# Kernel tuning notes

Hardware: AMD Instinct MI355X
Metric: run time of the kernel (lower is better)

## Reference

```python
import jax, jax.numpy as jnp
import numpy as np

EPS = 1e-6
N_HEADS = 16


def _inner(x, y):
    # Lorentzian inner product: -x0*y0 + <x_space, y_space>
    return -x[..., 0] * y[..., 0] + jnp.sum(x[..., 1:] * y[..., 1:], axis=-1)


def _project(x):
    sp = jnp.clip(x[..., 1:], -8.0, 8.0)
    x0 = jnp.sqrt(1.0 + jnp.sum(sp ** 2, axis=-1, keepdims=True) + EPS)
    return jnp.concatenate([x0, sp], axis=-1)


def _exp_map(x, v):
    vx = _inner(v, x)[..., None]
    v_tan = v + vx * x
    v_ns = jnp.maximum(_inner(v_tan, v_tan), 0.0)
    v_n = jnp.minimum(jnp.sqrt(v_ns + EPS)[..., None], 5.0)
    res = jnp.cosh(v_n) * x + jnp.sinh(v_n) * v_tan / (v_n + EPS)
    return _project(res)


def _log_map(x, y):
    y = _project(y)
    xy = jnp.minimum(_inner(x, y)[..., None], -(1.0 + EPS))
    d = jnp.maximum(jnp.arccosh(jnp.maximum(-xy, 1.0 + EPS)), 0.001)
    direc = y + xy * x
    dn = jnp.sqrt(jnp.maximum(_inner(direc, direc), EPS))[..., None]
    return d * direc / (dn + EPS)


def setup_inputs() -> dict:
    key = jax.random.key(0)
    ks = jax.random.split(key, 5)
    B, T, d = 2, 1024, 1024
    x = jax.random.normal(ks[0], (B, T, d), dtype=jnp.float32)
    s = 0.02
    Wq = jax.random.normal(ks[1], (d, d), dtype=jnp.float32) * s
    Wk = jax.random.normal(ks[2], (d, d), dtype=jnp.float32) * s
    Wv = jax.random.normal(ks[3], (d, d), dtype=jnp.float32) * s
    Wo = jax.random.normal(ks[4], (d, d), dtype=jnp.float32) * s
    return {"x": x, "Wq": Wq, "Wk": Wk, "Wv": Wv, "Wo": Wo}


def reference(x, Wq, Wk, Wv, Wo):
    B, T, d = x.shape
    h = N_HEADS
    dh = d // h
    mu = jnp.zeros((d,), dtype=x.dtype).at[0].set(1.0)  # hyperboloid origin

    v = _log_map(mu, x)  # [B, T, d]

    def proj_h(w):
        hh = w.reshape(B, T, h, dh)
        sp = jnp.clip(hh[..., 1:], -5.0, 5.0)
        x0 = jnp.sqrt(1.0 + jnp.sum(sp ** 2, axis=-1, keepdims=True) + EPS)
        return jnp.transpose(jnp.concatenate([x0, sp], axis=-1), (0, 2, 1, 3))  # [B,h,T,dh]

    q = proj_h(v @ Wq.T)
    k = proj_h(v @ Wk.T)
    vv = jnp.transpose((v @ Wv.T).reshape(B, T, h, dh), (0, 2, 1, 3))  # [B,h,T,dh]

    # Lorentzian scores: -q0*k0 + <q_space, k_space>
    sc = (-jnp.einsum("bhqi,bhki->bhqk", q[..., :1], k[..., :1])
          + jnp.einsum("bhqc,bhkc->bhqk", q[..., 1:], k[..., 1:])) / (dh ** 0.5)
    at = jax.nn.softmax(sc, axis=-1)
    out = jnp.einsum("bhqk,bhkc->bhqc", at, vv)
    out = jnp.transpose(out, (0, 2, 1, 3)).reshape(B, T, d)
    return _project(_exp_map(mu, out @ Wo.T))
```

## Files before the change

kernel.cpp:

```cpp
#include <hip/hip_runtime.h>

#define EPSF 1e-6f

typedef __bf16 bf16x8 __attribute__((ext_vector_type(8)));
typedef float f32x4 __attribute__((ext_vector_type(4)));
typedef __attribute__((address_space(3))) unsigned int as3_uint;
typedef __attribute__((address_space(1))) const unsigned int as1_uint;

__device__ __forceinline__ unsigned short f2bf(float f) {
  unsigned int u = __builtin_bit_cast(unsigned int, f);
  u += 0x7fffu + ((u >> 16) & 1u);
  return (unsigned short)(u >> 16);
}
__device__ __forceinline__ float bf2f(unsigned short u) {
  unsigned int v = (unsigned int)u << 16;
  return __builtin_bit_cast(float, v);
}

__global__ __launch_bounds__(256) void prep_and_conv(
    const float* __restrict__ x, const float* __restrict__ Wq,
    const float* __restrict__ Wk, const float* __restrict__ Wv,
    const float* __restrict__ Wo, unsigned short* __restrict__ vbf,
    unsigned short* __restrict__ wqk, unsigned short* __restrict__ wvb,
    unsigned short* __restrict__ wob) {
  int bid = blockIdx.x;
  int tid = threadIdx.x;
  if (bid >= 2048) {
    int t = bid - 2048;
    int y = t >> 10;
    const float* src = (y == 0) ? Wq : (y == 1) ? Wk : (y == 2) ? Wv : Wo;
    unsigned short* dst = (y == 0) ? wqk : (y == 1) ? wqk + 1048576
                          : (y == 2) ? wvb : wob;
    int i = (t & 1023) * 256 + tid;
    f32x4 v = ((const f32x4*)src)[i];
    ushort4 o;
    o.x = f2bf(v[0]); o.y = f2bf(v[1]); o.z = f2bf(v[2]); o.w = f2bf(v[3]);
    ((ushort4*)dst)[i] = o;
    return;
  }
  int row = bid;
  const float* xr = x + (size_t)row * 1024;
  float vals[4];
  float ssq = 0.f;
#pragma unroll
  for (int i = 0; i < 4; ++i) {
    int c = tid + i * 256;
    float t = xr[c];
    if (c == 0) {
      vals[i] = 0.f;
    } else {
      t = fminf(fmaxf(t, -8.f), 8.f);
      vals[i] = t;
      ssq += t * t;
    }
  }
#pragma unroll
  for (int off = 32; off; off >>= 1) ssq += __shfl_xor(ssq, off);
  __shared__ float red[4];
  int wv = tid >> 6;
  if ((tid & 63) == 0) red[wv] = ssq;
  __syncthreads();
  ssq = red[0] + red[1] + red[2] + red[3];

  float y0 = sqrtf(1.f + ssq + EPSF);
  float xy = fminf(-y0, -(1.f + EPSF));
  float mxy = fmaxf(-xy, 1.f + EPSF);
  float dd = fmaxf(acoshf(mxy), 0.001f);
  float d0 = y0 + xy;
  float inn = ssq - d0 * d0;
  float dn = sqrtf(fmaxf(inn, EPSF));
  float inv = dd / (dn + EPSF);

  unsigned short* vr = vbf + (size_t)row * 1024;
#pragma unroll
  for (int i = 0; i < 4; ++i) {
    int c = tid + i * 256;
    float o = (c == 0) ? d0 * inv : vals[i] * inv;
    vr[c] = f2bf(o);
  }
}

__device__ __forceinline__ void gemm128_body(
    const unsigned short* __restrict__ A, const unsigned short* __restrict__ Bw,
    int K, int row0, int col0, unsigned short* As, unsigned short* Bs,
    f32x4 (*acc)[4]) {
  int tid = threadIdx.x;
  int lane = tid & 63, w = tid >> 6;
  int wm = (w >> 1) * 64, wn = (w & 1) * 64;
  int lq = lane & 15, g = lane >> 4;
  const unsigned short* Ag =
      A + (size_t)(row0 + w * 8 + (lane >> 3)) * K + (lane & 7) * 8;
  const unsigned short* Bg =
      Bw + (size_t)(col0 + w * 8 + (lane >> 3)) * K + (lane & 7) * 8;

  for (int k0 = 0; k0 < K; k0 += 64) {
    __syncthreads();
#pragma unroll
    for (int it = 0; it < 4; ++it) {
      __builtin_amdgcn_global_load_lds(
          (as1_uint*)(Ag + (size_t)(it * 32) * K + k0),
          (as3_uint*)&As[(it * 32 + w * 8) * 64], 16, 0, 0);
      __builtin_amdgcn_global_load_lds(
          (as1_uint*)(Bg + (size_t)(it * 32) * K + k0),
          (as3_uint*)&Bs[(it * 32 + w * 8) * 64], 16, 0, 0);
    }
    __syncthreads();
#pragma unroll
    for (int ks = 0; ks < 2; ++ks) {
      bf16x8 af[4], bfr[4];
#pragma unroll
      for (int i = 0; i < 4; ++i)
        af[i] = *(const bf16x8*)&As[(wm + i * 16 + lq) * 64 + ks * 32 + g * 8];
#pragma unroll
      for (int j = 0; j < 4; ++j)
        bfr[j] = *(const bf16x8*)&Bs[(wn + j * 16 + lq) * 64 + ks * 32 + g * 8];
#pragma unroll
      for (int i = 0; i < 4; ++i)
#pragma unroll
        for (int j = 0; j < 4; ++j)
          acc[i][j] =
              __builtin_amdgcn_mfma_f32_16x16x32_bf16(af[i], bfr[j], acc[i][j], 0, 0, 0);
    }
  }
}

__global__ __launch_bounds__(256) void gemm_qkv(
    const unsigned short* __restrict__ vbf, const unsigned short* __restrict__ wqk,
    const unsigned short* __restrict__ wvb, unsigned short* __restrict__ qb,
    unsigned short* __restrict__ kb, unsigned short* __restrict__ vtb) {
  __shared__ unsigned short As[128 * 64];
  __shared__ unsigned short Bs[128 * 64];
  f32x4 acc[4][4] = {};
  int tid = threadIdx.x;
  int lane = tid & 63, w = tid >> 6;
  int wm = (w >> 1) * 64, wn = (w & 1) * 64;
  int lq = lane & 15, g = lane >> 4;
  int bid = blockIdx.x;

  if (bid < 256) {
    int row0 = (bid & 15) * 128, col0 = (bid >> 4) * 128;
    gemm128_body(vbf, wqk, 1024, row0, col0, As, Bs, acc);
    int headg = (col0 + wn) >> 6;
    int qmode = (headg < 16) ? 1 : 0;
    unsigned short* dst = qmode ? qb : kb;
    size_t colb = (size_t)(headg & 15) * 64;
    float scale = qmode ? 0.125f : 1.f;
#pragma unroll
    for (int i = 0; i < 4; ++i)
#pragma unroll
      for (int r = 0; r < 4; ++r) {
        float s = 0.f;
#pragma unroll
        for (int j = 0; j < 4; ++j) {
          float vc = fminf(fmaxf(acc[i][j][r], -5.f), 5.f);
          s += (j == 0 && lq == 0) ? 0.f : vc * vc;
        }
        s += __shfl_xor(s, 1);
        s += __shfl_xor(s, 2);
        s += __shfl_xor(s, 4);
        s += __shfl_xor(s, 8);
        float x0 = sqrtf(1.f + s + EPSF);
        int row = row0 + wm + i * 16 + g * 4 + r;
#pragma unroll
        for (int j = 0; j < 4; ++j) {
          float vc = fminf(fmaxf(acc[i][j][r], -5.f), 5.f);
          float o = (j == 0 && lq == 0) ? (qmode ? -x0 : x0) : vc;
          dst[(size_t)row * 1024 + colb + j * 16 + lq] = f2bf(o * scale);
        }
      }
  } else {
    int t = bid - 256;
    int row0 = (t & 7) * 128, col0 = (t >> 3) * 128;
    gemm128_body(wvb, vbf, 1024, row0, col0, As, Bs, acc);
#pragma unroll
    for (int i = 0; i < 4; ++i)
#pragma unroll
      for (int j = 0; j < 4; ++j)
#pragma unroll
        for (int r = 0; r < 4; ++r)
          vtb[(size_t)(row0 + wm + i * 16 + g * 4 + r) * 2048 + col0 + wn + j * 16 + lq] =
              f2bf(acc[i][j][r]);
  }
}

__global__ __launch_bounds__(256) void gemm_wo(
    const unsigned short* __restrict__ A, const unsigned short* __restrict__ Bw,
    unsigned short* __restrict__ C) {
  __shared__ unsigned short As[128 * 64];
  __shared__ unsigned short Bs[128 * 64];
  f32x4 acc[4][4] = {};
  int bid = blockIdx.x;
  int row0 = (bid & 15) * 128, col0 = (bid >> 4) * 128;
  gemm128_body(A, Bw, 1024, row0, col0, As, Bs, acc);
  int tid = threadIdx.x;
  int lane = tid & 63, w = tid >> 6;
  int wm = (w >> 1) * 64, wn = (w & 1) * 64;
  int lq = lane & 15, g = lane >> 4;
#pragma unroll
  for (int i = 0; i < 4; ++i)
#pragma unroll
    for (int j = 0; j < 4; ++j)
#pragma unroll
      for (int r = 0; r < 4; ++r)
        C[(size_t)(row0 + wm + i * 16 + g * 4 + r) * 1024 + col0 + wn + j * 16 + lq] =
            f2bf(acc[i][j][r]);
}

__global__ __launch_bounds__(256) void attn_mfma(
    const unsigned short* __restrict__ Qb, const unsigned short* __restrict__ Kb,
    const unsigned short* __restrict__ Vtb, unsigned short* __restrict__ Obf) {
  __shared__ unsigned short Ks[2][64 * 64];
  __shared__ unsigned short Vs[2][64 * 64];
  __shared__ unsigned short Ps[4 * 16 * 64];
  int tid = threadIdx.x;
  int lane = tid & 63, w = tid >> 6;
  int g = lane >> 4, lq = lane & 15;
  int bh = blockIdx.x >> 4, qt = blockIdx.x & 15;
  int b = bh >> 4, h = bh & 15;

  const unsigned short* qrow =
      Qb + (size_t)(b * 1024 + qt * 64 + w * 16 + lq) * 1024 + h * 64;
  bf16x8 qf0 = *(const bf16x8*)(qrow + g * 8);
  bf16x8 qf1 = *(const bf16x8*)(qrow + 32 + g * 8);

  float mreg = -1e30f, lreg = 0.f;
  f32x4 acc[4] = {};
  unsigned short* Pw = Ps + w * 16 * 64;
  int sx = 8 * (lq & 7);

  const unsigned short* Ksrc = Kb + (size_t)(b * 1024) * 1024 + h * 64;
  const unsigned short* Vsrc = Vtb + (size_t)(h * 64) * 2048 + b * 1024;

  int srow = lane >> 3;
  int scg = (lane & 7) ^ srow;
  const unsigned short* Kp = Ksrc + (size_t)(w * 8 + srow) * 1024 + scg * 8;
  const unsigned short* Vp = Vsrc + (size_t)(w * 8 + srow) * 2048 + scg * 8;

  auto stage = [&](int buf, int kt) {
#pragma unroll
    for (int it = 0; it < 2; ++it) {
      __builtin_amdgcn_global_load_lds(
          (as1_uint*)(Kp + (size_t)(kt * 64 + it * 32) * 1024),
          (as3_uint*)&Ks[buf][(it * 32 + w * 8) * 64], 16, 0, 0);
      __builtin_amdgcn_global_load_lds(
          (as1_uint*)(Vp + (size_t)(it * 32) * 2048 + kt * 64),
          (as3_uint*)&Vs[buf][(it * 32 + w * 8) * 64], 16, 0, 0);
    }
  };

  auto compute = [&](int buf) {
    f32x4 st[4];
#pragma unroll
    for (int i = 0; i < 4; ++i) {
      int ro = i * 16 + lq;
      int rb = ro * 64, xx = 8 * (ro & 7);
      bf16x8 a0 = *(const bf16x8*)&Ks[buf][rb + ((g * 8) ^ xx)];
      bf16x8 a1 = *(const bf16x8*)&Ks[buf][rb + ((32 + g * 8) ^ xx)];
      f32x4 z = {};
      z = __builtin_amdgcn_mfma_f32_16x16x32_bf16(a0, qf0, z, 0, 0, 0);
      st[i] = __builtin_amdgcn_mfma_f32_16x16x32_bf16(a1, qf1, z, 0, 0, 0);
    }
    float pmax = st[0][0];
#pragma unroll
    for (int i = 0; i < 4; ++i)
#pragma unroll
      for (int r = 0; r < 4; ++r) pmax = fmaxf(pmax, st[i][r]);
    pmax = fmaxf(pmax, __shfl_xor(pmax, 16));
    pmax = fmaxf(pmax, __shfl_xor(pmax, 32));
    float nm = fmaxf(mreg, pmax);
    float sc_ = __expf(mreg - nm);
    mreg = nm;
    float ps = 0.f;
#pragma unroll
    for (int i = 0; i < 4; ++i) {
      ushort4 pq;
      float p0 = __expf(st[i][0] - nm);
      float p1 = __expf(st[i][1] - nm);
      float p2 = __expf(st[i][2] - nm);
      float p3 = __expf(st[i][3] - nm);
      ps += (p0 + p1) + (p2 + p3);
      pq.x = f2bf(p0); pq.y = f2bf(p1); pq.z = f2bf(p2); pq.w = f2bf(p3);
      *(ushort4*)&Pw[lq * 64 + ((g * 4 + i * 16) ^ sx)] = pq;
    }
    ps += __shfl_xor(ps, 16);
    ps += __shfl_xor(ps, 32);
    lreg = lreg * sc_ + ps;

    float scr[4];
#pragma unroll
    for (int r = 0; r < 4; ++r) scr[r] = __shfl(sc_, g * 4 + r);
#pragma unroll
    for (int jj = 0; jj < 4; ++jj)
#pragma unroll
      for (int r = 0; r < 4; ++r) acc[jj][r] *= scr[r];
#pragma unroll
    for (int ks = 0; ks < 2; ++ks) {
      bf16x8 pa = *(const bf16x8*)&Pw[lq * 64 + ((ks * 32 + g * 8) ^ sx)];
#pragma unroll
      for (int jj = 0; jj < 4; ++jj) {
        int vr = 16 * jj + lq;
        bf16x8 vb = *(const bf16x8*)&Vs[buf][vr * 64 + ((ks * 32 + g * 8) ^ (8 * (vr & 7)))];
        acc[jj] = __builtin_amdgcn_mfma_f32_16x16x32_bf16(pa, vb, acc[jj], 0, 0, 0);
      }
    }
  };

  stage(0, 0);
  int buf = 0;
  for (int kt = 0; kt < 16; ++kt) {
    __syncthreads();
    if (kt + 1 < 16) stage(buf ^ 1, kt + 1);
    compute(buf);
    buf ^= 1;
  }

  float linv = 1.f / lreg;
  float ilr[4];
#pragma unroll
  for (int r = 0; r < 4; ++r) ilr[r] = __shfl(linv, g * 4 + r);
  unsigned short* obase =
      Obf + (size_t)(b * 1024 + qt * 64 + w * 16) * 1024 + h * 64;
#pragma unroll
  for (int r = 0; r < 4; ++r)
#pragma unroll
    for (int jj = 0; jj < 4; ++jj)
      obase[(size_t)(g * 4 + r) * 1024 + 16 * jj + lq] = f2bf(acc[jj][r] * ilr[r]);
}

__global__ __launch_bounds__(256) void expmap_project(
    const unsigned short* __restrict__ c2, float* __restrict__ out) {
  int row = blockIdx.x;
  int tid = threadIdx.x;
  const unsigned short* cr = c2 + (size_t)row * 1024;
  float vals[4];
  float ssq = 0.f;
#pragma unroll
  for (int i = 0; i < 4; ++i) {
    int c = tid + i * 256;
    float t = bf2f(cr[c]);
    vals[i] = (c == 0) ? 0.f : t;
    ssq += vals[i] * vals[i];
  }
#pragma unroll
  for (int off = 32; off; off >>= 1) ssq += __shfl_xor(ssq, off);
  __shared__ float red1[4], red2[4];
  int wv = tid >> 6;
  if ((tid & 63) == 0) red1[wv] = ssq;
  __syncthreads();
  ssq = red1[0] + red1[1] + red1[2] + red1[3];
  float vn = fminf(sqrtf(ssq + EPSF), 5.f);
  float bf = sinhf(vn) / (vn + EPSF);
  float s2 = 0.f;
#pragma unroll
  for (int i = 0; i < 4; ++i) {
    float r = fminf(fmaxf(bf * vals[i], -8.f), 8.f);
    vals[i] = r;
    s2 += r * r;
  }
#pragma unroll
  for (int off = 32; off; off >>= 1) s2 += __shfl_xor(s2, off);
  if ((tid & 63) == 0) red2[wv] = s2;
  __syncthreads();
  s2 = red2[0] + red2[1] + red2[2] + red2[3];
  float x0 = sqrtf(1.f + s2 + EPSF);
  float* orow = out + (size_t)row * 1024;
#pragma unroll
  for (int i = 0; i < 4; ++i) {
    int c = tid + i * 256;
    orow[c] = (c == 0) ? x0 : vals[i];
  }
}

extern "C" void kernel_launch(void* const* d_in, const int* in_sizes, int n_in,
                              void* d_out, int out_size, void* d_ws, size_t ws_size,
                              hipStream_t stream) {
  (void)in_sizes; (void)n_in; (void)out_size; (void)ws_size;
  const float* x  = (const float*)d_in[0];
  const float* Wq = (const float*)d_in[1];
  const float* Wk = (const float*)d_in[2];
  const float* Wv = (const float*)d_in[3];
  const float* Wo = (const float*)d_in[4];
  float* out = (float*)d_out;

  char* w = (char*)d_ws;
  unsigned short* vbf = (unsigned short*)w; w += (size_t)2048 * 1024 * 2;
  unsigned short* wqk = (unsigned short*)w; w += (size_t)2048 * 1024 * 2;
  unsigned short* wvb = (unsigned short*)w; w += (size_t)1024 * 1024 * 2;
  unsigned short* wob = (unsigned short*)w; w += (size_t)1024 * 1024 * 2;
  unsigned short* vtb = (unsigned short*)w; w += (size_t)1024 * 2048 * 2;
  unsigned short* qb  = (unsigned short*)w; w += (size_t)2048 * 1024 * 2;
  unsigned short* kb  = (unsigned short*)w; w += (size_t)2048 * 1024 * 2;
  unsigned short* aob = (unsigned short*)w; w += (size_t)2048 * 1024 * 2;
  unsigned short* c2  = (unsigned short*)w; w += (size_t)2048 * 1024 * 2;

  prep_and_conv<<<6144, 256, 0, stream>>>(x, Wq, Wk, Wv, Wo, vbf, wqk, wvb, wob);

  gemm_qkv<<<384, 256, 0, stream>>>(vbf, wqk, wvb, qb, kb, vtb);

  attn_mfma<<<512, 256, 0, stream>>>(qb, kb, vtb, aob);

  gemm_wo<<<128, 256, 0, stream>>>(aob, wob, c2);
  expmap_project<<<2048, 256, 0, stream>>>(c2, out);
}
```

Measured before the change: 93.23 us.

## Retile Wo GEMM to 128x64, lazy softmax rescale, setprio and block remap in attention

```diff
diff --git a/kernel.cpp b/kernel.cpp
--- a/kernel.cpp
+++ b/kernel.cpp
@@ -187,19 +187,52 @@
     const unsigned short* __restrict__ A, const unsigned short* __restrict__ Bw,
     unsigned short* __restrict__ C) {
   __shared__ unsigned short As[128 * 64];
-  __shared__ unsigned short Bs[128 * 64];
-  f32x4 acc[4][4] = {};
-  int bid = blockIdx.x;
-  int row0 = (bid & 15) * 128, col0 = (bid >> 4) * 128;
-  gemm128_body(A, Bw, 1024, row0, col0, As, Bs, acc);
+  __shared__ unsigned short Bs[64 * 64];
   int tid = threadIdx.x;
   int lane = tid & 63, w = tid >> 6;
-  int wm = (w >> 1) * 64, wn = (w & 1) * 64;
+  int wm = (w >> 1) * 64, wn = (w & 1) * 32;
   int lq = lane & 15, g = lane >> 4;
+  int row0 = (blockIdx.x & 15) * 128, col0 = (blockIdx.x >> 4) * 64;
+  f32x4 acc[4][2] = {};
+  const unsigned short* Ag =
+      A + (size_t)(row0 + w * 8 + (lane >> 3)) * 1024 + (lane & 7) * 8;
+  const unsigned short* Bg =
+      Bw + (size_t)(col0 + w * 8 + (lane >> 3)) * 1024 + (lane & 7) * 8;
+
+  for (int k0 = 0; k0 < 1024; k0 += 64) {
+    __syncthreads();
+#pragma unroll
+    for (int it = 0; it < 4; ++it)
+      __builtin_amdgcn_global_load_lds(
+          (as1_uint*)(Ag + (size_t)(it * 32) * 1024 + k0),
+          (as3_uint*)&As[(it * 32 + w * 8) * 64], 16, 0, 0);
+#pragma unroll
+    for (int it = 0; it < 2; ++it)
+      __builtin_amdgcn_global_load_lds(
+          (as1_uint*)(Bg + (size_t)(it * 32) * 1024 + k0),
+          (as3_uint*)&Bs[(it * 32 + w * 8) * 64], 16, 0, 0);
+    __syncthreads();
+#pragma unroll
+    for (int ks = 0; ks < 2; ++ks) {
+      bf16x8 af[4], bfr[2];
+#pragma unroll
+      for (int i = 0; i < 4; ++i)
+        af[i] = *(const bf16x8*)&As[(wm + i * 16 + lq) * 64 + ks * 32 + g * 8];
+#pragma unroll
+      for (int j = 0; j < 2; ++j)
+        bfr[j] = *(const bf16x8*)&Bs[(wn + j * 16 + lq) * 64 + ks * 32 + g * 8];
+#pragma unroll
+      for (int i = 0; i < 4; ++i)
+#pragma unroll
+        for (int j = 0; j < 2; ++j)
+          acc[i][j] =
+              __builtin_amdgcn_mfma_f32_16x16x32_bf16(af[i], bfr[j], acc[i][j], 0, 0, 0);
+    }
+  }
 #pragma unroll
   for (int i = 0; i < 4; ++i)
 #pragma unroll
-    for (int j = 0; j < 4; ++j)
+    for (int j = 0; j < 2; ++j)
 #pragma unroll
       for (int r = 0; r < 4; ++r)
         C[(size_t)(row0 + wm + i * 16 + g * 4 + r) * 1024 + col0 + wn + j * 16 + lq] =
@@ -215,7 +248,10 @@
   int tid = threadIdx.x;
   int lane = tid & 63, w = tid >> 6;
   int g = lane >> 4, lq = lane & 15;
-  int bh = blockIdx.x >> 4, qt = blockIdx.x & 15;
+  int bid = blockIdx.x;
+  int idx = bid >> 3;
+  int bh = (bid & 7) * 4 + (idx & 3);
+  int qt = idx >> 2;
   int b = bh >> 4, h = bh & 15;
 
   const unsigned short* qrow =
@@ -250,6 +286,7 @@
 
   auto compute = [&](int buf) {
     f32x4 st[4];
+    __builtin_amdgcn_s_setprio(1);
 #pragma unroll
     for (int i = 0; i < 4; ++i) {
       int ro = i * 16 + lq;
@@ -260,6 +297,7 @@
       z = __builtin_amdgcn_mfma_f32_16x16x32_bf16(a0, qf0, z, 0, 0, 0);
       st[i] = __builtin_amdgcn_mfma_f32_16x16x32_bf16(a1, qf1, z, 0, 0, 0);
     }
+    __builtin_amdgcn_s_setprio(0);
     float pmax = st[0][0];
 #pragma unroll
     for (int i = 0; i < 4; ++i)
@@ -267,32 +305,36 @@
       for (int r = 0; r < 4; ++r) pmax = fmaxf(pmax, st[i][r]);
     pmax = fmaxf(pmax, __shfl_xor(pmax, 16));
     pmax = fmaxf(pmax, __shfl_xor(pmax, 32));
-    float nm = fmaxf(mreg, pmax);
-    float sc_ = __expf(mreg - nm);
-    mreg = nm;
+    if (__any(pmax > mreg + 8.f)) {
+      float nm = fmaxf(mreg, pmax);
+      float sc_ = __expf(mreg - nm);
+      mreg = nm;
+      lreg *= sc_;
+      float scr[4];
+#pragma unroll
+      for (int r = 0; r < 4; ++r) scr[r] = __shfl(sc_, g * 4 + r);
+#pragma unroll
+      for (int jj = 0; jj < 4; ++jj)
+#pragma unroll
+        for (int r = 0; r < 4; ++r) acc[jj][r] *= scr[r];
+    }
     float ps = 0.f;
 #pragma unroll
     for (int i = 0; i < 4; ++i) {
       ushort4 pq;
-      float p0 = __expf(st[i][0] - nm);
-      float p1 = __expf(st[i][1] - nm);
-      float p2 = __expf(st[i][2] - nm);
-      float p3 = __expf(st[i][3] - nm);
+      float p0 = __expf(st[i][0] - mreg);
+      float p1 = __expf(st[i][1] - mreg);
+      float p2 = __expf(st[i][2] - mreg);
+      float p3 = __expf(st[i][3] - mreg);
       ps += (p0 + p1) + (p2 + p3);
       pq.x = f2bf(p0); pq.y = f2bf(p1); pq.z = f2bf(p2); pq.w = f2bf(p3);
       *(ushort4*)&Pw[lq * 64 + ((g * 4 + i * 16) ^ sx)] = pq;
     }
     ps += __shfl_xor(ps, 16);
     ps += __shfl_xor(ps, 32);
-    lreg = lreg * sc_ + ps;
-
-    float scr[4];
-#pragma unroll
-    for (int r = 0; r < 4; ++r) scr[r] = __shfl(sc_, g * 4 + r);
-#pragma unroll
-    for (int jj = 0; jj < 4; ++jj)
-#pragma unroll
-      for (int r = 0; r < 4; ++r) acc[jj][r] *= scr[r];
+    lreg += ps;
+
+    __builtin_amdgcn_s_setprio(1);
 #pragma unroll
     for (int ks = 0; ks < 2; ++ks) {
       bf16x8 pa = *(const bf16x8*)&Pw[lq * 64 + ((ks * 32 + g * 8) ^ sx)];
@@ -303,6 +345,7 @@
         acc[jj] = __builtin_amdgcn_mfma_f32_16x16x32_bf16(pa, vb, acc[jj], 0, 0, 0);
       }
     }
+    __builtin_amdgcn_s_setprio(0);
   };
 
   stage(0, 0);
@@ -399,6 +442,6 @@
 
   attn_mfma<<<512, 256, 0, stream>>>(qb, kb, vtb, aob);
 
-  gemm_wo<<<128, 256, 0, stream>>>(aob, wob, c2);
+  gemm_wo<<<256, 256, 0, stream>>>(aob, wob, c2);
   expmap_project<<<2048, 256, 0, stream>>>(c2, out);
 }
```

Result: faster. 84.78 us (-9.1%).
